# Kernel tuning notes

Measured on AMD Instinct MI355X. Metric: run time of the kernel, lower is better.

The kernel has to match this reference:

```python
import jax, jax.numpy as jnp
import numpy as np

K, T, CIN = 30000, 35, 7
EPS = 1e-5  # torch BatchNorm default


def _bn(x, gamma, beta):
    # x: [1, K, T, C]; per-channel batch-stat normalization over (0,1,2)
    mean = jnp.mean(x, axis=(0, 1, 2))
    var = jnp.var(x, axis=(0, 1, 2))
    return (x - mean) * jax.lax.rsqrt(var + EPS) * gamma + beta


def _vfe(x, mask, W, b, gamma, beta):
    # x: [1, K, T, Cin] -> [1, K, T, 2*units]
    pw = jnp.einsum('bkti,iu->bktu', x, W) + b
    pw = jax.nn.relu(_bn(pw, gamma, beta))
    agg = jnp.max(pw, axis=2, keepdims=True)            # [1, K, 1, units]
    out = jnp.concatenate([pw, jnp.broadcast_to(agg, pw.shape)], axis=-1)
    return out * mask


def setup_inputs() -> dict:
    key = jax.random.key(0)
    ks = jax.random.split(key, 8)
    inp = {}
    inp['x'] = jax.random.normal(ks[0], (K, T, CIN), jnp.float32)
    inp['coordinate'] = jax.random.randint(ks[1], (K, 4), 0, 1, dtype=jnp.int32)
    inp['batch_size'] = 1
    inp['W1'] = jax.random.normal(ks[2], (7, 16), jnp.float32) * 0.3
    inp['b1'] = jnp.zeros((16,), jnp.float32)
    inp['g1'] = jnp.ones((16,), jnp.float32)
    inp['be1'] = jnp.zeros((16,), jnp.float32)
    inp['W2'] = jax.random.normal(ks[3], (32, 64), jnp.float32) * 0.15
    inp['b2'] = jnp.zeros((64,), jnp.float32)
    inp['g2'] = jnp.ones((64,), jnp.float32)
    inp['be2'] = jnp.zeros((64,), jnp.float32)
    inp['Wd'] = jax.random.normal(ks[4], (128, 128), jnp.float32) * 0.1
    inp['bd'] = jnp.zeros((128,), jnp.float32)
    inp['gd'] = jnp.ones((128,), jnp.float32)
    inp['bed'] = jnp.zeros((128,), jnp.float32)
    return inp


def reference(x, coordinate, batch_size, W1, b1, g1, be1, W2, b2, g2, be2, Wd, bd, gd, bed):
    xb = x[None]                                   # [1, K, T, 7]
    # mask: 1 where the point's feature sum is nonzero
    mask = (jnp.sum(xb, axis=-1) != 0.0).astype(jnp.float32)[..., None]  # [1,K,T,1]
    h = _vfe(xb, mask, W1, b1, g1, be1)            # [1, K, T, 32]
    h = _vfe(h, mask, W2, b2, g2, be2)             # [1, K, T, 128]
    h = jnp.einsum('bktc,cd->bktd', h, Wd) + bd    # [1, K, T, 128]
    h = _bn(h, gd, bed)                            # BatchNorm2d after permute(0,3,1,2)
    h = jnp.where(h >= 0, h, 0.1 * h)              # leaky_relu(0.1)
    h = jnp.max(h, axis=2)                         # max over points -> [1, K, 128]
    out = jnp.transpose(h, (0, 2, 1))              # [1, 128, K] to match NCHW layout
    return (out, coordinate)
```

## Files before the change

### kernel.cpp

```cpp
#include <hip/hip_runtime.h>

#define KVOX 30000
#define TP 35
#define NPTS (KVOX * TP)
#define EPS_BN 1e-5f

typedef __attribute__((ext_vector_type(8))) short short8_t;
typedef __attribute__((ext_vector_type(4))) float f32x4;
typedef __attribute__((ext_vector_type(2))) float f32x2;

#define MFMA_BF16 __builtin_amdgcn_mfma_f32_16x16x32_bf16

#define SLOTG_OFF 0
#define SLOT2_OFF 2560
#define SLOT3_OFF 10752
#define PAR_A1 27136
#define PAR_C1 27152
#define PAR_A2 27168
#define PAR_C2 27232
#define PAR_A3 27296
#define PAR_C3 27424
#define STATS_FLOATS 27136
#define W2T_OFF 27552
#define WDT_OFF 28576
#define M3_OFF 36768
#define SMALL_FLOATS (36768 + KVOX * 64)
#define H1G_OFF SMALL_FLOATS
#define REC_DW 696
#define FULL_FLOATS (H1G_OFF + (KVOX / 2) * REC_DW)

__device__ __forceinline__ ushort f2bf(float f) {
    uint r;
    asm("v_cvt_pk_bf16_f32 %0, %1, %2" : "=v"(r) : "v"(f), "v"(f));
    return (ushort)r;
}
__device__ __forceinline__ uint f2bf2(float lo, float hi) {
    uint r;
    asm("v_cvt_pk_bf16_f32 %0, %1, %2" : "=v"(r) : "v"(lo), "v"(hi));
    return r;
}
__device__ __forceinline__ float bf2f(ushort h) {
    union { uint u; float f; } v; v.u = ((uint)h) << 16; return v.f;
}
__device__ __forceinline__ f32x2 mk2(float a, float b) {
    f32x2 r; r[0] = a; r[1] = b; return r;
}

__global__ __launch_bounds__(256) void k_prep_stats1(
    const float* __restrict__ x,
    const float* __restrict__ W2, const float* __restrict__ Wd,
    const float* __restrict__ gd,
    ushort* __restrict__ w2t, ushort* __restrict__ wdt,
    float* __restrict__ slotG) {
    if (blockIdx.x < 64) {
        int t = blockIdx.x * 256 + threadIdx.x;
        if (t < 2048) {
            int u = t >> 5, k = t & 31;
            w2t[t] = f2bf(W2[k * 64 + u]);
        }
        int u = t >> 7, k = t & 127;
        float sg = (gd[u] < 0.f) ? -1.f : 1.f;
        wdt[t] = f2bf(Wd[k * 128 + u] * sg);
        return;
    }
    int bid = blockIdx.x - 64;
    int tid = threadIdx.x;
    int gid = bid * 256 + tid;
    float sx[7], G[28];
#pragma unroll
    for (int c = 0; c < 7; ++c) sx[c] = 0.f;
#pragma unroll
    for (int i = 0; i < 28; ++i) G[i] = 0.f;
    for (int p = gid; p < NPTS; p += 256 * 256) {
        const float* xp = x + (size_t)p * 7;
        float xv[7];
#pragma unroll
        for (int c = 0; c < 7; ++c) { xv[c] = xp[c]; sx[c] += xv[c]; }
        int idx = 0;
#pragma unroll
        for (int i = 0; i < 7; ++i)
#pragma unroll
            for (int j = i; j < 7; ++j) { G[idx] = fmaf(xv[i], xv[j], G[idx]); ++idx; }
    }
    int lane = tid & 63;
    int wv = tid >> 6;
    int slot = (bid * 4 + wv) & 63;
#pragma unroll
    for (int k = 0; k < 35; ++k) {
        float v = (k < 28) ? G[k] : sx[k - 28];
#pragma unroll
        for (int m = 32; m > 0; m >>= 1) v += __shfl_xor(v, m, 64);
        if (lane == 0) atomicAdd(&slotG[slot * 40 + k], v);
    }
}

__global__ void k_affine1g(const float* __restrict__ slotG,
                           const float* __restrict__ W1, const float* __restrict__ b1,
                           const float* __restrict__ g1, const float* __restrict__ be1,
                           float* __restrict__ pa, float* __restrict__ pc, float invN) {
    __shared__ float red[35];
    int t = threadIdx.x;
    if (t < 35) {
        float s = 0.f;
#pragma unroll
        for (int sl = 0; sl < 64; ++sl) s += slotG[sl * 40 + t];
        red[t] = s;
    }
    __syncthreads();
    if (t < 16) {
        float wv[7];
#pragma unroll
        for (int c = 0; c < 7; ++c) wv[c] = W1[c * 16 + t];
        float b = b1[t];
        float sw = 0.f;
#pragma unroll
        for (int c = 0; c < 7; ++c) sw = fmaf(red[28 + c], wv[c], sw);
        float gq = 0.f;
        int idx = 0;
#pragma unroll
        for (int i = 0; i < 7; ++i)
#pragma unroll
            for (int j = i; j < 7; ++j) {
                float coef = wv[i] * wv[j];
                if (i != j) coef *= 2.f;
                gq = fmaf(coef, red[idx], gq);
                ++idx;
            }
        float mr = sw * invN;
        float mean = mr + b;
        float ex2 = gq * invN + 2.f * b * mr + b * b;
        float var = ex2 - mean * mean;
        float av = g1[t] * rsqrtf(var + EPS_BN);
        pa[t] = av;
        pc[t] = be1[t] - mean * av;
    }
}

__global__ void k_affine_b(const float* __restrict__ slots,
                           const float* __restrict__ g,
                           const float* __restrict__ be,
                           const float* __restrict__ bias,
                           float* __restrict__ pa, float* __restrict__ pc,
                           int C, float invN) {
    int u = threadIdx.x;
    if (u >= C) return;
    float s = 0.f, q = 0.f;
    for (int sl = 0; sl < 64; ++sl) {
        s += slots[sl * 2 * C + u];
        q += slots[sl * 2 * C + C + u];
    }
    float b = bias[u];
    float mr = s * invN;
    float mean = mr + b;
    float ex2 = q * invN + 2.f * b * mr + b * b;
    float var = ex2 - mean * mean;
    float av = g[u] * rsqrtf(var + EPS_BN);
    pa[u] = av;
    pc[u] = be[u] - mean * av;
}

__global__ void k_affine_b3(const float* __restrict__ slots,
                            const float* __restrict__ g,
                            const float* __restrict__ be,
                            const float* __restrict__ bias,
                            float* __restrict__ pa, float* __restrict__ pc,
                            int C, float invN) {
    int u = threadIdx.x;
    if (u >= C) return;
    float s = 0.f, q = 0.f;
    for (int sl = 0; sl < 64; ++sl) {
        s += slots[sl * 2 * C + u];
        q += slots[sl * 2 * C + C + u];
    }
    float sg = (g[u] < 0.f) ? -1.f : 1.f;
    s *= sg;
    float b = bias[u];
    float mr = s * invN;
    float mean = mr + b;
    float ex2 = q * invN + 2.f * b * mr + b * b;
    float var = ex2 - mean * mean;
    float av = g[u] * rsqrtf(var + EPS_BN);
    pa[u] = av;
    pc[u] = be[u] - mean * av;
}

__device__ __forceinline__ void phaseA_il(
    int k0, int tid,
    const float* __restrict__ x,
    const float* __restrict__ W1, const float* __restrict__ b1,
    const float* __restrict__ a1, const float* __restrict__ c1,
    ushort* __restrict__ h1, float* __restrict__ lmask,
    float* __restrict__ aggp, ushort* __restrict__ agg1bf) {
    int u = tid & 15;
    int g = tid >> 4;
    int v = g & 1;
    int th = g >> 1;
    float pmax = 0.f;
    if (th < 7) {
        float b1u = b1[u];
        float a1u = a1[u], c1u = c1[u];
        float w1c[7];
#pragma unroll
        for (int c = 0; c < 7; ++c) w1c[c] = W1[c * 16 + u];
#pragma unroll
        for (int i = 0; i < 5; ++i) {
            int t = th * 5 + i;
            const float* xp = x + ((size_t)(k0 + v) * TP + t) * 7;
            float xv[7];
            float sum7 = 0.f;
#pragma unroll
            for (int c = 0; c < 7; ++c) { xv[c] = xp[c]; sum7 += xv[c]; }
            float mkv = (sum7 != 0.f) ? 1.f : 0.f;
            int row = 2 * t + v;
            if (u == 0) lmask[row] = mkv;
            float val = b1u;
#pragma unroll
            for (int c = 0; c < 7; ++c) val = fmaf(xv[c], w1c[c], val);
            val = fmaxf(fmaf(a1u, val, c1u), 0.f);
            pmax = fmaxf(pmax, val);
            h1[row * 24 + u] = f2bf(val * mkv);
        }
    } else if (g < 16) {
#pragma unroll
        for (int i = 0; i < 5; ++i) {
            int row = 70 + (g & 1) + 2 * i;
            h1[row * 24 + u] = 0;
            if (u == 0) lmask[row] = 0.f;
        }
    }
    pmax = fmaxf(pmax, __shfl_xor(pmax, 32, 64));
    int w = tid >> 6;
    int lane = tid & 63;
    if (lane < 32 && w < 4) aggp[w * 32 + lane] = pmax;
    __syncthreads();
    if (tid < 16) {
        float g0 = fmaxf(fmaxf(aggp[u], aggp[32 + u]),
                         fmaxf(aggp[64 + u], aggp[96 + u]));
        float g1 = fmaxf(fmaxf(aggp[16 + u], aggp[48 + u]),
                         fmaxf(aggp[80 + u], aggp[112 + u]));
        agg1bf[u] = f2bf(g0);
        agg1bf[16 + u] = f2bf(g1);
    }
    __syncthreads();
}

template <bool DUMP>
__global__ __launch_bounds__(256, 8) void k_stats2(
    const float* __restrict__ x,
    const float* __restrict__ W1, const float* __restrict__ b1,
    const ushort* __restrict__ w2t,
    const float* __restrict__ ws,
    float* __restrict__ slot2, uint* __restrict__ recs) {
    __shared__ __align__(16) ushort h1[80 * 24];
    __shared__ float lmask[80];
    __shared__ float aggp[128];
    __shared__ __align__(16) ushort agg1bf[32];
    __shared__ __align__(16) uint zeros16[4];
    int tid = threadIdx.x;
    int k0 = blockIdx.x * 2;
    if (tid < 4) zeros16[tid] = 0;
    phaseA_il(k0, tid, x, W1, b1, ws + PAR_A1, ws + PAR_C1, h1, lmask, aggp, agg1bf);
    if (DUMP) {
        uint* rec = recs + (size_t)blockIdx.x * REC_DW;
        const uint* h1dw = (const uint*)h1;
        for (int i = tid; i < 640; i += 256) rec[i] = h1dw[(i >> 3) * 12 + (i & 7)];
        if (tid < 16) rec[640 + tid] = ((const uint*)agg1bf)[tid];
        if (tid < 40) rec[656 + tid] = f2bf2(lmask[2 * tid], lmask[2 * tid + 1]);
    }
    int w = tid >> 6, lane = tid & 63, lq = lane >> 4, lr = lane & 15;
    int u = w * 16 + lr;
    short8_t bB = *(const short8_t*)(w2t + u * 32 + (lq & 1) * 8);
    const ushort* pa = (lq < 2) ? (agg1bf + (lr & 1) * 16 + lq * 8) : (const ushort*)zeros16;
    short8_t pAf = *(const short8_t*)pa;
    short8_t bP = *(const short8_t*)(w2t + u * 32 + 16 + (lq & 1) * 8);
    f32x4 aP = {0.f, 0.f, 0.f, 0.f};
    aP = MFMA_BF16(pAf, bP, aP, 0, 0, 0);
    f32x2 p1p = mk2(__shfl(aP[0], lr, 64), __shfl(aP[1], lr, 64));
    f32x2 s1p = {0.f, 0.f}, s2p = {0.f, 0.f};
#pragma unroll
    for (int mt = 0; mt < 5; ++mt) {
        const ushort* ha = (lq < 2) ? (h1 + (mt * 16 + lr) * 24 + lq * 8) : (const ushort*)zeros16;
        short8_t af = *(const short8_t*)ha;
        f32x4 acc = {0.f, 0.f, 0.f, 0.f};
        acc = MFMA_BF16(af, bB, acc, 0, 0, 0);
        const f32x4 mk = *(const f32x4*)(lmask + mt * 16 + lq * 4);
        f32x2 am01 = (mk2(acc[0], acc[1]) + p1p) * mk2(mk[0], mk[1]);
        f32x2 am23 = (mk2(acc[2], acc[3]) + p1p) * mk2(mk[2], mk[3]);
        s1p += am01 + am23;
        s2p += am01 * am01;
        s2p += am23 * am23;
    }
    float s1 = s1p[0] + s1p[1], s2 = s2p[0] + s2p[1];
    s1 += __shfl_xor(s1, 16, 64); s1 += __shfl_xor(s1, 32, 64);
    s2 += __shfl_xor(s2, 16, 64); s2 += __shfl_xor(s2, 32, 64);
    if (lq == 0) {
        int slot = blockIdx.x & 63;
        atomicAdd(&slot2[slot * 128 + u], s1);
        atomicAdd(&slot2[slot * 128 + 64 + u], s2);
    }
}

__global__ __launch_bounds__(512, 8) void k_stage3_reuse(
    const uint* __restrict__ recs,
    const float* __restrict__ b2,
    const ushort* __restrict__ w2t, const ushort* __restrict__ wdt,
    const float* __restrict__ bd, const float* __restrict__ gd,
    const float* __restrict__ ws,
    float* __restrict__ slot3, ushort* __restrict__ m3) {
    __shared__ __align__(16) ushort h1[80 * 24];
    __shared__ __align__(16) ushort h2[80 * 72];
    __shared__ float lmask[80];
    __shared__ float aggh[2][2][64];
    __shared__ __align__(16) ushort agg1bf[32];
    __shared__ __align__(16) ushort agg2bf[2 * 64];
    __shared__ __align__(16) uint zeros16[4];
    int tid = threadIdx.x;
    int k0 = blockIdx.x * 2;
    int w = tid >> 6, lane = tid & 63, lq = lane >> 4, lr = lane & 15;

    {
        const uint* rec = recs + (size_t)blockIdx.x * REC_DW;
        uint* h1dw = (uint*)h1;
        h1dw[(tid >> 3) * 12 + (tid & 7)] = rec[tid];
        if (tid < 184) {
            int i2 = 512 + tid;
            if (i2 < 640) h1dw[(i2 >> 3) * 12 + (i2 & 7)] = rec[i2];
            else if (i2 < 656) ((uint*)agg1bf)[i2 - 640] = rec[i2];
            else {
                uint mw = rec[i2];
                int j = i2 - 656;
                lmask[2 * j] = bf2f((ushort)(mw & 0xffffu));
                lmask[2 * j + 1] = bf2f((ushort)(mw >> 16));
            }
        }
        if (tid < 4) zeros16[tid] = 0;
    }
    __syncthreads();

    {
        int mh = w >> 2, uq = w & 3;
        int u = uq * 16 + lr;
        short8_t bB = *(const short8_t*)(w2t + u * 32 + (lq & 1) * 8);
        const ushort* pa = (lq < 2) ? (agg1bf + (lr & 1) * 16 + lq * 8) : (const ushort*)zeros16;
        short8_t pAf = *(const short8_t*)pa;
        short8_t bP = *(const short8_t*)(w2t + u * 32 + 16 + (lq & 1) * 8);
        f32x4 aP = {0.f, 0.f, 0.f, 0.f};
        aP = MFMA_BF16(pAf, bP, aP, 0, 0, 0);
        f32x2 p1p = mk2(__shfl(aP[0], lr, 64), __shfl(aP[1], lr, 64));
        float a2u = ws[PAR_A2 + u];
        float c2u = fmaf(a2u, b2[u], ws[PAR_C2 + u]);
        f32x2 a2p = mk2(a2u, a2u), c2p = mk2(c2u, c2u);
        float av0 = 0.f, av1 = 0.f;
        int mt0 = mh ? 3 : 0, mt1 = mh ? 5 : 3;
        for (int mt = mt0; mt < mt1; ++mt) {
            const ushort* ha = (lq < 2) ? (h1 + (mt * 16 + lr) * 24 + lq * 8) : (const ushort*)zeros16;
            short8_t af = *(const short8_t*)ha;
            f32x4 acc = {0.f, 0.f, 0.f, 0.f};
            acc = MFMA_BF16(af, bB, acc, 0, 0, 0);
            const f32x4 mk = *(const f32x4*)(lmask + mt * 16 + lq * 4);
            int m0 = mt * 16 + lq * 4;
            f32x2 am01 = (mk2(acc[0], acc[1]) + p1p) * mk2(mk[0], mk[1]);
            f32x2 am23 = (mk2(acc[2], acc[3]) + p1p) * mk2(mk[2], mk[3]);
            f32x2 t01 = a2p * am01 + c2p;
            f32x2 t23 = a2p * am23 + c2p;
            float v0 = fmaxf(t01[0], 0.f), v1 = fmaxf(t01[1], 0.f);
            float v2 = fmaxf(t23[0], 0.f), v3 = fmaxf(t23[1], 0.f);
            h2[(m0 + 0) * 72 + u] = f2bf(v0);
            h2[(m0 + 1) * 72 + u] = f2bf(v1);
            h2[(m0 + 2) * 72 + u] = f2bf(v2);
            h2[(m0 + 3) * 72 + u] = f2bf(v3);
            if (mt == 4) {
                bool c01 = lq < 2, c23 = lq < 1;
                v0 = c01 ? v0 : 0.f; v1 = c01 ? v1 : 0.f;
                v2 = c23 ? v2 : 0.f; v3 = c23 ? v3 : 0.f;
            }
            av0 = fmaxf(av0, fmaxf(v0, v2));
            av1 = fmaxf(av1, fmaxf(v1, v3));
        }
        av0 = fmaxf(av0, __shfl_xor(av0, 16, 64));
        av0 = fmaxf(av0, __shfl_xor(av0, 32, 64));
        av1 = fmaxf(av1, __shfl_xor(av1, 16, 64));
        av1 = fmaxf(av1, __shfl_xor(av1, 32, 64));
        if (lq == 0) { aggh[mh][0][u] = av0; aggh[mh][1][u] = av1; }
    }
    __syncthreads();
    if (tid < 32) {
        int u2 = tid;
        float l0 = fmaxf(aggh[0][0][2 * u2], aggh[1][0][2 * u2]);
        float h0 = fmaxf(aggh[0][0][2 * u2 + 1], aggh[1][0][2 * u2 + 1]);
        float l1 = fmaxf(aggh[0][1][2 * u2], aggh[1][1][2 * u2]);
        float h1v = fmaxf(aggh[0][1][2 * u2 + 1], aggh[1][1][2 * u2 + 1]);
        ((uint*)agg2bf)[u2] = f2bf2(l0, h0);
        ((uint*)agg2bf)[32 + u2] = f2bf2(l1, h1v);
    }
    __syncthreads();

    {
        int u = w * 16 + lr;
        short8_t bM0 = *(const short8_t*)(wdt + u * 128 + lq * 8);
        short8_t bM1 = *(const short8_t*)(wdt + u * 128 + 32 + lq * 8);
        short8_t bP0 = *(const short8_t*)(wdt + u * 128 + 64 + lq * 8);
        short8_t bP1 = *(const short8_t*)(wdt + u * 128 + 96 + lq * 8);
        short8_t pA0 = *(const short8_t*)(agg2bf + (lr & 1) * 64 + lq * 8);
        short8_t pA1 = *(const short8_t*)(agg2bf + (lr & 1) * 64 + 32 + lq * 8);
        f32x4 aP = {0.f, 0.f, 0.f, 0.f};
        aP = MFMA_BF16(pA0, bP0, aP, 0, 0, 0);
        aP = MFMA_BF16(pA1, bP1, aP, 0, 0, 0);
        f32x2 p2p = mk2(__shfl(aP[0], lr, 64), __shfl(aP[1], lr, 64));
        float mx0 = -1e30f, mx1 = -1e30f;
        f32x2 s1p = {0.f, 0.f}, s2p = {0.f, 0.f};
#pragma unroll
        for (int mt = 0; mt < 5; ++mt) {
            const ushort* hrow = h2 + (mt * 16 + lr) * 72;
            short8_t a0 = *(const short8_t*)(hrow + lq * 8);
            short8_t a1 = *(const short8_t*)(hrow + 32 + lq * 8);
            f32x4 acc = {0.f, 0.f, 0.f, 0.f};
            acc = MFMA_BF16(a0, bM0, acc, 0, 0, 0);
            acc = MFMA_BF16(a1, bM1, acc, 0, 0, 0);
            const f32x4 mk = *(const f32x4*)(lmask + mt * 16 + lq * 4);
            f32x2 am01 = (mk2(acc[0], acc[1]) + p2p) * mk2(mk[0], mk[1]);
            f32x2 am23 = (mk2(acc[2], acc[3]) + p2p) * mk2(mk[2], mk[3]);
            s1p += am01 + am23;
            s2p += am01 * am01;
            s2p += am23 * am23;
            if (mt < 4) {
                mx0 = fmaxf(mx0, fmaxf(am01[0], am23[0]));
                mx1 = fmaxf(mx1, fmaxf(am01[1], am23[1]));
            } else {
                bool c01 = lq < 2, c23 = lq < 1;
                mx0 = fmaxf(mx0, fmaxf(c01 ? am01[0] : -1e30f, c23 ? am23[0] : -1e30f));
                mx1 = fmaxf(mx1, fmaxf(c01 ? am01[1] : -1e30f, c23 ? am23[1] : -1e30f));
            }
        }
        mx0 = fmaxf(mx0, __shfl_xor(mx0, 16, 64));
        mx0 = fmaxf(mx0, __shfl_xor(mx0, 32, 64));
        mx1 = fmaxf(mx1, __shfl_xor(mx1, 16, 64));
        mx1 = fmaxf(mx1, __shfl_xor(mx1, 32, 64));
        float s1 = s1p[0] + s1p[1], s2 = s2p[0] + s2p[1];
        s1 += __shfl_xor(s1, 16, 64); s1 += __shfl_xor(s1, 32, 64);
        s2 += __shfl_xor(s2, 16, 64); s2 += __shfl_xor(s2, 32, 64);
        if (lq == 0) {
            float sg = (gd[u] < 0.f) ? -1.f : 1.f;
            float bdu = bd[u];
            m3[(size_t)k0 * 128 + u] = f2bf(fmaf(sg, mx0, bdu));
            m3[(size_t)(k0 + 1) * 128 + u] = f2bf(fmaf(sg, mx1, bdu));
            int slot = blockIdx.x & 63;
            atomicAdd(&slot3[slot * 256 + u], s1);
            atomicAdd(&slot3[slot * 256 + 128 + u], s2);
        }
    }
}

__device__ __forceinline__ void phaseA_leg(
    int k0, int tid,
    const float* __restrict__ x,
    const float* __restrict__ W1, const float* __restrict__ b1,
    const float* __restrict__ a1, const float* __restrict__ c1,
    ushort* __restrict__ h1, float* __restrict__ lmask, float* __restrict__ aggp) {
    int u = tid & 15;
    int g = tid >> 4;
    int v = g & 1;
    int th = g >> 1;
    float pmax = 0.f;
    if (th < 7) {
        float b1u = b1[u];
        float a1u = a1[u], c1u = c1[u];
        float w1c[7];
#pragma unroll
        for (int c = 0; c < 7; ++c) w1c[c] = W1[c * 16 + u];
#pragma unroll
        for (int i = 0; i < 5; ++i) {
            int t = th * 5 + i;
            const float* xp = x + ((size_t)(k0 + v) * TP + t) * 7;
            float xv[7];
            float sum7 = 0.f;
#pragma unroll
            for (int c = 0; c < 7; ++c) { xv[c] = xp[c]; sum7 += xv[c]; }
            float mkv = (sum7 != 0.f) ? 1.f : 0.f;
            if (u == 0) lmask[v * TP + t] = mkv;
            float val = b1u;
#pragma unroll
            for (int c = 0; c < 7; ++c) val = fmaf(xv[c], w1c[c], val);
            val = fmaxf(fmaf(a1u, val, c1u), 0.f);
            pmax = fmaxf(pmax, val);
            h1[(v * TP + t) * 40 + u] = f2bf(val * mkv);
        }
    } else {
#pragma unroll
        for (int i = 0; i < 5; ++i) {
            int row = 70 + (g & 1) * 5 + i;
            h1[row * 40 + u] = 0;
            if (u == 0) lmask[row] = 0.f;
        }
    }
    pmax = fmaxf(pmax, __shfl_xor(pmax, 32, 64));
    int w = tid >> 6;
    int lane = tid & 63;
    if (lane < 32) aggp[w * 32 + lane] = pmax;
    __syncthreads();
    {
        int uu = tid & 15;
        int r0 = tid >> 4;
        float g0 = fmaxf(fmaxf(aggp[uu], aggp[32 + uu]),
                         fmaxf(aggp[64 + uu], aggp[96 + uu]));
        float g1 = fmaxf(fmaxf(aggp[16 + uu], aggp[48 + uu]),
                         fmaxf(aggp[80 + uu], aggp[112 + uu]));
        ushort a0 = f2bf(g0), a1b = f2bf(g1);
#pragma unroll
        for (int j = 0; j < 5; ++j) {
            int row = r0 + j * 16;
            float mkv = lmask[row];
            h1[row * 40 + 16 + uu] = (mkv != 0.f) ? ((row < TP) ? a0 : a1b) : (ushort)0;
        }
    }
    __syncthreads();
}

template <bool WSPATH>
__global__ __launch_bounds__(256) void k_stage3_full(
    const float* __restrict__ x,
    const float* __restrict__ W1, const float* __restrict__ b1,
    const float* __restrict__ b2,
    const ushort* __restrict__ w2t, const ushort* __restrict__ wdt,
    const float* __restrict__ bd, const float* __restrict__ gd,
    const float* __restrict__ ws,
    float* __restrict__ slot3,
    ushort* __restrict__ m3, float* __restrict__ outbuf) {
    __shared__ __align__(16) ushort h1[80 * 40];
    __shared__ __align__(16) ushort h2[80 * 136];
    __shared__ float lmask[80];
    __shared__ float aggp[128];
    __shared__ ushort agg2bf[128];
    int tid = threadIdx.x;
    int k0 = blockIdx.x * 2;
    int w = tid >> 6, lane = tid & 63, lq = lane >> 4, lr = lane & 15;
    phaseA_leg(k0, tid, x, W1, b1, ws + PAR_A1, ws + PAR_C1, h1, lmask, aggp);

    int u0 = w * 32;
    short8_t bfr[2][4];
#pragma unroll
    for (int s = 0; s < 2; ++s)
#pragma unroll
        for (int kk = 0; kk < 4; ++kk)
            bfr[s][kk] = *(const short8_t*)(wdt + ((u0 + s * 16 + lr) * 128 + kk * 32 + lq * 8));

    {
        int u = w * 16 + lr;
        short8_t bfrag = *(const short8_t*)(w2t + u * 32 + lq * 8);
        float a2u = ws[PAR_A2 + u];
        float c2p = fmaf(a2u, b2[u], ws[PAR_C2 + u]);
        float aggv0 = 0.f, aggv1 = 0.f;
#pragma unroll
        for (int mt = 0; mt < 5; ++mt) {
            short8_t afrag = *(const short8_t*)(h1 + (mt * 16 + lr) * 40 + lq * 8);
            f32x4 acc = {0.f, 0.f, 0.f, 0.f};
            acc = MFMA_BF16(afrag, bfrag, acc, 0, 0, 0);
#pragma unroll
            for (int r = 0; r < 4; ++r) {
                int m = mt * 16 + lq * 4 + r;
                float val = fmaxf(fmaf(a2u, acc[r], c2p), 0.f);
                float vm = (m < 70) ? val : 0.f;
                if (m < TP) aggv0 = fmaxf(aggv0, vm); else aggv1 = fmaxf(aggv1, vm);
                h2[m * 136 + u] = f2bf(val * lmask[m]);
            }
        }
        aggv0 = fmaxf(aggv0, __shfl_xor(aggv0, 16, 64));
        aggv0 = fmaxf(aggv0, __shfl_xor(aggv0, 32, 64));
        aggv1 = fmaxf(aggv1, __shfl_xor(aggv1, 16, 64));
        aggv1 = fmaxf(aggv1, __shfl_xor(aggv1, 32, 64));
        if (lq == 0) {
            agg2bf[u] = f2bf(aggv0);
            agg2bf[64 + u] = f2bf(aggv1);
        }
    }
    __syncthreads();
    {
        int c = tid & 63;
        int r0 = tid >> 6;
        ushort a0 = agg2bf[c], a1v = agg2bf[64 + c];
#pragma unroll
        for (int j = 0; j < 20; ++j) {
            int row = r0 + j * 4;
            float mkv = lmask[row];
            h2[row * 136 + 64 + c] = (mkv != 0.f) ? ((row < TP) ? a0 : a1v) : (ushort)0;
        }
    }
    __syncthreads();
    {
        float mxa[2][2], s1a[2], s2a[2];
#pragma unroll
        for (int s = 0; s < 2; ++s) {
            s1a[s] = 0.f; s2a[s] = 0.f;
            mxa[s][0] = -1e30f; mxa[s][1] = -1e30f;
        }
#pragma unroll
        for (int mt = 0; mt < 5; ++mt) {
            short8_t af[4];
#pragma unroll
            for (int kk = 0; kk < 4; ++kk)
                af[kk] = *(const short8_t*)(h2 + (mt * 16 + lr) * 136 + kk * 32 + lq * 8);
#pragma unroll
            for (int s = 0; s < 2; ++s) {
                f32x4 acc = {0.f, 0.f, 0.f, 0.f};
#pragma unroll
                for (int kk = 0; kk < 4; ++kk)
                    acc = MFMA_BF16(af[kk], bfr[s][kk], acc, 0, 0, 0);
#pragma unroll
                for (int r = 0; r < 4; ++r) {
                    float a = acc[r];
                    s1a[s] += a;
                    s2a[s] = fmaf(a, a, s2a[s]);
                    int m = mt * 16 + lq * 4 + r;
                    if (mt <= 1) mxa[s][0] = fmaxf(mxa[s][0], a);
                    else if (mt == 3) mxa[s][1] = fmaxf(mxa[s][1], a);
                    else if (mt == 2) { if (m < TP) mxa[s][0] = fmaxf(mxa[s][0], a); else mxa[s][1] = fmaxf(mxa[s][1], a); }
                    else { if (m < 70) mxa[s][1] = fmaxf(mxa[s][1], a); }
                }
            }
        }
#pragma unroll
        for (int s = 0; s < 2; ++s) {
#pragma unroll
            for (int v = 0; v < 2; ++v) {
                mxa[s][v] = fmaxf(mxa[s][v], __shfl_xor(mxa[s][v], 16, 64));
                mxa[s][v] = fmaxf(mxa[s][v], __shfl_xor(mxa[s][v], 32, 64));
            }
            s1a[s] += __shfl_xor(s1a[s], 16, 64); s1a[s] += __shfl_xor(s1a[s], 32, 64);
            s2a[s] += __shfl_xor(s2a[s], 16, 64); s2a[s] += __shfl_xor(s2a[s], 32, 64);
        }
        if (lq == 0) {
            int slot = blockIdx.x & 63;
#pragma unroll
            for (int s = 0; s < 2; ++s) {
                int u = u0 + s * 16 + lr;
                float bdu = bd[u];
                float sg = (gd[u] < 0.f) ? -1.f : 1.f;
#pragma unroll
                for (int v = 0; v < 2; ++v) {
                    float res = fmaf(sg, mxa[s][v], bdu);
                    if (WSPATH) m3[(size_t)(k0 + v) * 128 + u] = f2bf(res);
                    else        outbuf[(size_t)u * KVOX + (k0 + v)] = res;
                }
                atomicAdd(&slot3[slot * 256 + u], s1a[s]);
                atomicAdd(&slot3[slot * 256 + 128 + u], s2a[s]);
            }
        }
    }
}

__global__ __launch_bounds__(256) void k_final_ws(const ushort* __restrict__ m3,
                                                  const float* __restrict__ ws,
                                                  float* __restrict__ out) {
    __shared__ float tile[32][33];
    int tx = threadIdx.x & 31;
    int ty = threadIdx.x >> 5;
    int v0 = blockIdx.x * 32;
    int u0 = blockIdx.y * 32;
    const float* a3 = ws + PAR_A3;
    const float* c3 = ws + PAR_C3;
#pragma unroll
    for (int r = ty; r < 32; r += 8) {
        int v = v0 + r, u = u0 + tx;
        float y = 0.f;
        if (v < KVOX) {
            float a = a3[u], c = c3[u];
            float val = bf2f(m3[(size_t)v * 128 + u]);
            y = a * val + c;
            y = (y >= 0.f) ? y : 0.1f * y;
        }
        tile[r][tx] = y;
    }
    __syncthreads();
#pragma unroll
    for (int r = ty; r < 32; r += 8) {
        int u = u0 + r, v = v0 + tx;
        if (v < KVOX) out[(size_t)u * KVOX + v] = tile[tx][r];
    }
}

__global__ __launch_bounds__(256) void k_final_inplace(const float* __restrict__ ws,
                                                       float* __restrict__ out) {
    int v = blockIdx.x * 256 + threadIdx.x;
    int u = blockIdx.y;
    if (v >= KVOX) return;
    float a = ws[PAR_A3 + u], c = ws[PAR_C3 + u];
    size_t idx = (size_t)u * KVOX + v;
    float y = a * out[idx] + c;
    out[idx] = (y >= 0.f) ? y : 0.1f * y;
}

extern "C" void kernel_launch(void* const* d_in, const int* in_sizes, int n_in,
                              void* d_out, int out_size, void* d_ws, size_t ws_size,
                              hipStream_t stream) {
    const float* x   = (const float*)d_in[0];
    const void*  coord = d_in[1];
    const float* W1  = (const float*)d_in[3];
    const float* b1  = (const float*)d_in[4];
    const float* g1  = (const float*)d_in[5];
    const float* be1 = (const float*)d_in[6];
    const float* W2  = (const float*)d_in[7];
    const float* b2  = (const float*)d_in[8];
    const float* g2  = (const float*)d_in[9];
    const float* be2 = (const float*)d_in[10];
    const float* Wd  = (const float*)d_in[11];
    const float* bd  = (const float*)d_in[12];
    const float* gd  = (const float*)d_in[13];
    const float* bed = (const float*)d_in[14];
    float* ws = (float*)d_ws;
    float* out = (float*)d_out;
    ushort* w2t = (ushort*)(ws + W2T_OFF);
    ushort* wdt = (ushort*)(ws + WDT_OFF);
    ushort* m3  = (ushort*)(ws + M3_OFF);
    uint* recs  = (uint*)(ws + H1G_OFF);

    size_t wsf = ws_size / 4;
    bool full = wsf >= (size_t)FULL_FLOATS;
    bool small = wsf >= (size_t)SMALL_FLOATS;
    const float invN = 1.f / (float)NPTS;

    hipMemsetAsync(d_ws, 0, (size_t)STATS_FLOATS * 4, stream);

    k_prep_stats1<<<64 + 256, 256, 0, stream>>>(x, W2, Wd, gd, w2t, wdt, ws + SLOTG_OFF);
    k_affine1g<<<1, 64, 0, stream>>>(ws + SLOTG_OFF, W1, b1, g1, be1, ws + PAR_A1, ws + PAR_C1, invN);
    if (full)
        k_stats2<true><<<KVOX / 2, 256, 0, stream>>>(x, W1, b1, w2t, ws, ws + SLOT2_OFF, recs);
    else
        k_stats2<false><<<KVOX / 2, 256, 0, stream>>>(x, W1, b1, w2t, ws, ws + SLOT2_OFF, recs);
    k_affine_b<<<1, 64, 0, stream>>>(ws + SLOT2_OFF, g2, be2, b2, ws + PAR_A2, ws + PAR_C2, 64, invN);

    if (full) {
        k_stage3_reuse<<<KVOX / 2, 512, 0, stream>>>(recs, b2, w2t, wdt, bd, gd, ws,
                                                     ws + SLOT3_OFF, m3);
        k_affine_b3<<<1, 128, 0, stream>>>(ws + SLOT3_OFF, gd, bed, bd, ws + PAR_A3, ws + PAR_C3, 128, invN);
        k_final_ws<<<dim3((KVOX + 31) / 32, 4), 256, 0, stream>>>(m3, ws, out);
    } else if (small) {
        k_stage3_full<true><<<KVOX / 2, 256, 0, stream>>>(x, W1, b1, b2, w2t, wdt, bd, gd, ws,
                                                          ws + SLOT3_OFF, m3, out);
        k_affine_b3<<<1, 128, 0, stream>>>(ws + SLOT3_OFF, gd, bed, bd, ws + PAR_A3, ws + PAR_C3, 128, invN);
        k_final_ws<<<dim3((KVOX + 31) / 32, 4), 256, 0, stream>>>(m3, ws, out);
    } else {
        k_stage3_full<false><<<KVOX / 2, 256, 0, stream>>>(x, W1, b1, b2, w2t, wdt, bd, gd, ws,
                                                           ws + SLOT3_OFF, m3, out);
        k_affine_b3<<<1, 128, 0, stream>>>(ws + SLOT3_OFF, gd, bed, bd, ws + PAR_A3, ws + PAR_C3, 128, invN);
        k_final_inplace<<<dim3((KVOX + 255) / 256, 128), 256, 0, stream>>>(ws, out);
    }
    hipMemcpyAsync((char*)d_out + (size_t)128 * KVOX * 4, coord,
                   (size_t)KVOX * 4 * sizeof(int), hipMemcpyDeviceToDevice, stream);
}
```

Before: 176.3 us.

## Process four voxels per block in stats2 and stage3 with full MFMA row use

Blocks in k_stats2 and k_stage3_reuse now handle four voxels (140 point rows padded to 144) instead of two. Each 16x16 MFMA tile therefore fills all four accumulator lanes rather than two, and the number of blocks is halved. The per-voxel max aggregation in stage 3 now goes through shared-memory atomicMax on float bits instead of a two-step reduction. Separately, the first-stage Gram statistics loop loads x as 16-byte vectors covering four points at once. The costs are larger shared-memory use per block, a bigger record layout, and reliance on the maxima being non-negative after ReLU so that atomicMax on float bits orders correctly.

```diff
diff --git a/kernel.cpp b/kernel.cpp
--- a/kernel.cpp
+++ b/kernel.cpp
@@ -7,7 +7,6 @@
 
 typedef __attribute__((ext_vector_type(8))) short short8_t;
 typedef __attribute__((ext_vector_type(4))) float f32x4;
-typedef __attribute__((ext_vector_type(2))) float f32x2;
 
 #define MFMA_BF16 __builtin_amdgcn_mfma_f32_16x16x32_bf16
 
@@ -26,8 +25,8 @@
 #define M3_OFF 36768
 #define SMALL_FLOATS (36768 + KVOX * 64)
 #define H1G_OFF SMALL_FLOATS
-#define REC_DW 696
-#define FULL_FLOATS (H1G_OFF + (KVOX / 2) * REC_DW)
+#define REC_DW 1224
+#define FULL_FLOATS (H1G_OFF + (KVOX / 4) * REC_DW)
 
 __device__ __forceinline__ ushort f2bf(float f) {
     uint r;
@@ -41,9 +40,6 @@
 }
 __device__ __forceinline__ float bf2f(ushort h) {
     union { uint u; float f; } v; v.u = ((uint)h) << 16; return v.f;
-}
-__device__ __forceinline__ f32x2 mk2(float a, float b) {
-    f32x2 r; r[0] = a; r[1] = b; return r;
 }
 
 __global__ __launch_bounds__(256) void k_prep_stats1(
@@ -71,16 +67,26 @@
     for (int c = 0; c < 7; ++c) sx[c] = 0.f;
 #pragma unroll
     for (int i = 0; i < 28; ++i) G[i] = 0.f;
-    for (int p = gid; p < NPTS; p += 256 * 256) {
-        const float* xp = x + (size_t)p * 7;
-        float xv[7];
-#pragma unroll
-        for (int c = 0; c < 7; ++c) { xv[c] = xp[c]; sx[c] += xv[c]; }
-        int idx = 0;
-#pragma unroll
-        for (int i = 0; i < 7; ++i)
-#pragma unroll
-            for (int j = i; j < 7; ++j) { G[idx] = fmaf(xv[i], xv[j], G[idx]); ++idx; }
+    for (size_t p4 = (size_t)gid * 4; p4 < NPTS; p4 += (size_t)65536 * 4) {
+        const f32x4* xp = (const f32x4*)(x + p4 * 7);
+        f32x4 q[7];
+#pragma unroll
+        for (int c = 0; c < 7; ++c) q[c] = xp[c];
+#pragma unroll
+        for (int j = 0; j < 4; ++j) {
+            float xv[7];
+#pragma unroll
+            for (int c = 0; c < 7; ++c) {
+                int idx = j * 7 + c;
+                xv[c] = q[idx >> 2][idx & 3];
+                sx[c] += xv[c];
+            }
+            int idx = 0;
+#pragma unroll
+            for (int i = 0; i < 7; ++i)
+#pragma unroll
+                for (int jj = i; jj < 7; ++jj) { G[idx] = fmaf(xv[i], xv[jj], G[idx]); ++idx; }
+        }
     }
     int lane = tid & 63;
     int wv = tid >> 6;
@@ -184,17 +190,17 @@
     pc[u] = be[u] - mean * av;
 }
 
-__device__ __forceinline__ void phaseA_il(
+__device__ __forceinline__ void phaseA4(
     int k0, int tid,
     const float* __restrict__ x,
     const float* __restrict__ W1, const float* __restrict__ b1,
     const float* __restrict__ a1, const float* __restrict__ c1,
     ushort* __restrict__ h1, float* __restrict__ lmask,
-    float* __restrict__ aggp, ushort* __restrict__ agg1bf) {
+    float* __restrict__ aggp , ushort* __restrict__ agg1bf ) {
     int u = tid & 15;
     int g = tid >> 4;
-    int v = g & 1;
-    int th = g >> 1;
+    int v = g & 3;
+    int th = g >> 2;
     float pmax = 0.f;
     if (th < 7) {
         float b1u = b1[u];
@@ -211,7 +217,7 @@
 #pragma unroll
             for (int c = 0; c < 7; ++c) { xv[c] = xp[c]; sum7 += xv[c]; }
             float mkv = (sum7 != 0.f) ? 1.f : 0.f;
-            int row = 2 * t + v;
+            int row = 4 * t + v;
             if (u == 0) lmask[row] = mkv;
             float val = b1u;
 #pragma unroll
@@ -220,77 +226,73 @@
             pmax = fmaxf(pmax, val);
             h1[row * 24 + u] = f2bf(val * mkv);
         }
-    } else if (g < 16) {
-#pragma unroll
-        for (int i = 0; i < 5; ++i) {
-            int row = 70 + (g & 1) + 2 * i;
-            h1[row * 24 + u] = 0;
-            if (u == 0) lmask[row] = 0.f;
-        }
-    }
-    pmax = fmaxf(pmax, __shfl_xor(pmax, 32, 64));
+    } else {
+        int row = 140 + v;
+        h1[row * 24 + u] = 0;
+        if (u == 0) lmask[row] = 0.f;
+    }
     int w = tid >> 6;
     int lane = tid & 63;
-    if (lane < 32 && w < 4) aggp[w * 32 + lane] = pmax;
-    __syncthreads();
-    if (tid < 16) {
-        float g0 = fmaxf(fmaxf(aggp[u], aggp[32 + u]),
-                         fmaxf(aggp[64 + u], aggp[96 + u]));
-        float g1 = fmaxf(fmaxf(aggp[16 + u], aggp[48 + u]),
-                         fmaxf(aggp[80 + u], aggp[112 + u]));
-        agg1bf[u] = f2bf(g0);
-        agg1bf[16 + u] = f2bf(g1);
+    if (w < 7) aggp[w * 64 + lane] = pmax;
+    __syncthreads();
+    if (tid < 64) {
+        float m = aggp[tid];
+#pragma unroll
+        for (int ww = 1; ww < 7; ++ww) m = fmaxf(m, aggp[ww * 64 + tid]);
+        agg1bf[tid] = f2bf(m);
     }
     __syncthreads();
 }
 
 template <bool DUMP>
-__global__ __launch_bounds__(256, 8) void k_stats2(
+__global__ __launch_bounds__(512, 8) void k_stats2(
     const float* __restrict__ x,
     const float* __restrict__ W1, const float* __restrict__ b1,
     const ushort* __restrict__ w2t,
     const float* __restrict__ ws,
     float* __restrict__ slot2, uint* __restrict__ recs) {
-    __shared__ __align__(16) ushort h1[80 * 24];
-    __shared__ float lmask[80];
-    __shared__ float aggp[128];
-    __shared__ __align__(16) ushort agg1bf[32];
+    __shared__ __align__(16) ushort h1[144 * 24];
+    __shared__ float lmask[144];
+    __shared__ float aggp[7 * 64];
+    __shared__ __align__(16) ushort agg1bf[64];
     __shared__ __align__(16) uint zeros16[4];
     int tid = threadIdx.x;
-    int k0 = blockIdx.x * 2;
+    int k0 = blockIdx.x * 4;
     if (tid < 4) zeros16[tid] = 0;
-    phaseA_il(k0, tid, x, W1, b1, ws + PAR_A1, ws + PAR_C1, h1, lmask, aggp, agg1bf);
+    phaseA4(k0, tid, x, W1, b1, ws + PAR_A1, ws + PAR_C1, h1, lmask, aggp, agg1bf);
     if (DUMP) {
         uint* rec = recs + (size_t)blockIdx.x * REC_DW;
         const uint* h1dw = (const uint*)h1;
-        for (int i = tid; i < 640; i += 256) rec[i] = h1dw[(i >> 3) * 12 + (i & 7)];
-        if (tid < 16) rec[640 + tid] = ((const uint*)agg1bf)[tid];
-        if (tid < 40) rec[656 + tid] = f2bf2(lmask[2 * tid], lmask[2 * tid + 1]);
+        for (int i = tid; i < 1120; i += 512) rec[i] = h1dw[(i >> 3) * 12 + (i & 7)];
+        if (tid < 32) rec[1120 + tid] = ((const uint*)agg1bf)[tid];
+        if (tid < 70) rec[1152 + tid] = f2bf2(lmask[2 * tid], lmask[2 * tid + 1]);
     }
     int w = tid >> 6, lane = tid & 63, lq = lane >> 4, lr = lane & 15;
-    int u = w * 16 + lr;
+    int mh = w >> 2, uq = w & 3;
+    int u = uq * 16 + lr;
     short8_t bB = *(const short8_t*)(w2t + u * 32 + (lq & 1) * 8);
-    const ushort* pa = (lq < 2) ? (agg1bf + (lr & 1) * 16 + lq * 8) : (const ushort*)zeros16;
-    short8_t pAf = *(const short8_t*)pa;
     short8_t bP = *(const short8_t*)(w2t + u * 32 + 16 + (lq & 1) * 8);
+    const ushort* pap = (lq < 2) ? (agg1bf + (lr & 3) * 16 + (lq & 1) * 8) : (const ushort*)zeros16;
+    short8_t pAf = *(const short8_t*)pap;
     f32x4 aP = {0.f, 0.f, 0.f, 0.f};
     aP = MFMA_BF16(pAf, bP, aP, 0, 0, 0);
-    f32x2 p1p = mk2(__shfl(aP[0], lr, 64), __shfl(aP[1], lr, 64));
-    f32x2 s1p = {0.f, 0.f}, s2p = {0.f, 0.f};
-#pragma unroll
-    for (int mt = 0; mt < 5; ++mt) {
-        const ushort* ha = (lq < 2) ? (h1 + (mt * 16 + lr) * 24 + lq * 8) : (const ushort*)zeros16;
+    f32x4 p1;
+    p1[0] = __shfl(aP[0], lr, 64); p1[1] = __shfl(aP[1], lr, 64);
+    p1[2] = __shfl(aP[2], lr, 64); p1[3] = __shfl(aP[3], lr, 64);
+    f32x4 s1p = {0.f, 0.f, 0.f, 0.f}, s2p = {0.f, 0.f, 0.f, 0.f};
+    int mt0 = mh ? 5 : 0, mt1 = mh ? 9 : 5;
+    for (int mt = mt0; mt < mt1; ++mt) {
+        const ushort* ha = (lq < 2) ? (h1 + (mt * 16 + lr) * 24 + (lq & 1) * 8) : (const ushort*)zeros16;
         short8_t af = *(const short8_t*)ha;
         f32x4 acc = {0.f, 0.f, 0.f, 0.f};
         acc = MFMA_BF16(af, bB, acc, 0, 0, 0);
-        const f32x4 mk = *(const f32x4*)(lmask + mt * 16 + lq * 4);
-        f32x2 am01 = (mk2(acc[0], acc[1]) + p1p) * mk2(mk[0], mk[1]);
-        f32x2 am23 = (mk2(acc[2], acc[3]) + p1p) * mk2(mk[2], mk[3]);
-        s1p += am01 + am23;
-        s2p += am01 * am01;
-        s2p += am23 * am23;
-    }
-    float s1 = s1p[0] + s1p[1], s2 = s2p[0] + s2p[1];
+        f32x4 mk = *(const f32x4*)(lmask + mt * 16 + lq * 4);
+        f32x4 am = (acc + p1) * mk;
+        s1p += am;
+        s2p += am * am;
+    }
+    float s1 = s1p[0] + s1p[1] + s1p[2] + s1p[3];
+    float s2 = s2p[0] + s2p[1] + s2p[2] + s2p[3];
     s1 += __shfl_xor(s1, 16, 64); s1 += __shfl_xor(s1, 32, 64);
     s2 += __shfl_xor(s2, 16, 64); s2 += __shfl_xor(s2, 32, 64);
     if (lq == 0) {
@@ -307,33 +309,38 @@
     const float* __restrict__ bd, const float* __restrict__ gd,
     const float* __restrict__ ws,
     float* __restrict__ slot3, ushort* __restrict__ m3) {
-    __shared__ __align__(16) ushort h1[80 * 24];
-    __shared__ __align__(16) ushort h2[80 * 72];
-    __shared__ float lmask[80];
-    __shared__ float aggh[2][2][64];
-    __shared__ __align__(16) ushort agg1bf[32];
-    __shared__ __align__(16) ushort agg2bf[2 * 64];
+    __shared__ __align__(16) ushort h1[144 * 24];
+    __shared__ __align__(16) ushort h2[144 * 72];
+    __shared__ float lmask[144];
+    __shared__ __align__(16) uint aggfU[4 * 68];
+    __shared__ __align__(16) ushort agg1bf[64];
     __shared__ __align__(16) uint zeros16[4];
     int tid = threadIdx.x;
-    int k0 = blockIdx.x * 2;
+    int k0 = blockIdx.x * 4;
     int w = tid >> 6, lane = tid & 63, lq = lane >> 4, lr = lane & 15;
 
     {
         const uint* rec = recs + (size_t)blockIdx.x * REC_DW;
         uint* h1dw = (uint*)h1;
-        h1dw[(tid >> 3) * 12 + (tid & 7)] = rec[tid];
-        if (tid < 184) {
-            int i2 = 512 + tid;
-            if (i2 < 640) h1dw[(i2 >> 3) * 12 + (i2 & 7)] = rec[i2];
-            else if (i2 < 656) ((uint*)agg1bf)[i2 - 640] = rec[i2];
-            else {
-                uint mw = rec[i2];
-                int j = i2 - 656;
-                lmask[2 * j] = bf2f((ushort)(mw & 0xffffu));
-                lmask[2 * j + 1] = bf2f((ushort)(mw >> 16));
-            }
-        }
-        if (tid < 4) zeros16[tid] = 0;
+        {
+            int i = tid;              h1dw[(i >> 3) * 12 + (i & 7)] = rec[i];
+            i = tid + 512;            h1dw[(i >> 3) * 12 + (i & 7)] = rec[i];
+            i = tid + 1024; if (i < 1120) h1dw[(i >> 3) * 12 + (i & 7)] = rec[i];
+        }
+        if (tid < 48) h1dw[140 * 12 + tid] = 0u;
+        if (tid < 32) ((uint*)agg1bf)[tid] = rec[1120 + tid];
+        if (tid < 72) {
+            if (tid < 70) {
+                uint mw = rec[1152 + tid];
+                lmask[2 * tid] = bf2f((ushort)(mw & 0xffffu));
+                lmask[2 * tid + 1] = bf2f((ushort)(mw >> 16));
+            } else {
+                int j = 140 + (tid - 70) * 2;
+                lmask[j] = 0.f; lmask[j + 1] = 0.f;
+            }
+        }
+        if (tid < 272) aggfU[tid] = 0u;
+        if (tid < 4) zeros16[tid] = 0u;
     }
     __syncthreads();
 
@@ -341,57 +348,48 @@
         int mh = w >> 2, uq = w & 3;
         int u = uq * 16 + lr;
         short8_t bB = *(const short8_t*)(w2t + u * 32 + (lq & 1) * 8);
-        const ushort* pa = (lq < 2) ? (agg1bf + (lr & 1) * 16 + lq * 8) : (const ushort*)zeros16;
-        short8_t pAf = *(const short8_t*)pa;
         short8_t bP = *(const short8_t*)(w2t + u * 32 + 16 + (lq & 1) * 8);
+        const ushort* pap = (lq < 2) ? (agg1bf + (lr & 3) * 16 + (lq & 1) * 8) : (const ushort*)zeros16;
+        short8_t pAf = *(const short8_t*)pap;
         f32x4 aP = {0.f, 0.f, 0.f, 0.f};
         aP = MFMA_BF16(pAf, bP, aP, 0, 0, 0);
-        f32x2 p1p = mk2(__shfl(aP[0], lr, 64), __shfl(aP[1], lr, 64));
+        f32x4 p1;
+        p1[0] = __shfl(aP[0], lr, 64); p1[1] = __shfl(aP[1], lr, 64);
+        p1[2] = __shfl(aP[2], lr, 64); p1[3] = __shfl(aP[3], lr, 64);
         float a2u = ws[PAR_A2 + u];
         float c2u = fmaf(a2u, b2[u], ws[PAR_C2 + u]);
-        f32x2 a2p = mk2(a2u, a2u), c2p = mk2(c2u, c2u);
-        float av0 = 0.f, av1 = 0.f;
-        int mt0 = mh ? 3 : 0, mt1 = mh ? 5 : 3;
+        f32x4 av = {0.f, 0.f, 0.f, 0.f};
+        int mt0 = mh ? 5 : 0, mt1 = mh ? 9 : 5;
         for (int mt = mt0; mt < mt1; ++mt) {
-            const ushort* ha = (lq < 2) ? (h1 + (mt * 16 + lr) * 24 + lq * 8) : (const ushort*)zeros16;
+            const ushort* ha = (lq < 2) ? (h1 + (mt * 16 + lr) * 24 + (lq & 1) * 8) : (const ushort*)zeros16;
             short8_t af = *(const short8_t*)ha;
             f32x4 acc = {0.f, 0.f, 0.f, 0.f};
             acc = MFMA_BF16(af, bB, acc, 0, 0, 0);
-            const f32x4 mk = *(const f32x4*)(lmask + mt * 16 + lq * 4);
+            f32x4 mk = *(const f32x4*)(lmask + mt * 16 + lq * 4);
             int m0 = mt * 16 + lq * 4;
-            f32x2 am01 = (mk2(acc[0], acc[1]) + p1p) * mk2(mk[0], mk[1]);
-            f32x2 am23 = (mk2(acc[2], acc[3]) + p1p) * mk2(mk[2], mk[3]);
-            f32x2 t01 = a2p * am01 + c2p;
-            f32x2 t23 = a2p * am23 + c2p;
-            float v0 = fmaxf(t01[0], 0.f), v1 = fmaxf(t01[1], 0.f);
-            float v2 = fmaxf(t23[0], 0.f), v3 = fmaxf(t23[1], 0.f);
-            h2[(m0 + 0) * 72 + u] = f2bf(v0);
-            h2[(m0 + 1) * 72 + u] = f2bf(v1);
-            h2[(m0 + 2) * 72 + u] = f2bf(v2);
-            h2[(m0 + 3) * 72 + u] = f2bf(v3);
-            if (mt == 4) {
-                bool c01 = lq < 2, c23 = lq < 1;
-                v0 = c01 ? v0 : 0.f; v1 = c01 ? v1 : 0.f;
-                v2 = c23 ? v2 : 0.f; v3 = c23 ? v3 : 0.f;
-            }
-            av0 = fmaxf(av0, fmaxf(v0, v2));
-            av1 = fmaxf(av1, fmaxf(v1, v3));
-        }
-        av0 = fmaxf(av0, __shfl_xor(av0, 16, 64));
-        av0 = fmaxf(av0, __shfl_xor(av0, 32, 64));
-        av1 = fmaxf(av1, __shfl_xor(av1, 16, 64));
-        av1 = fmaxf(av1, __shfl_xor(av1, 32, 64));
-        if (lq == 0) { aggh[mh][0][u] = av0; aggh[mh][1][u] = av1; }
-    }
-    __syncthreads();
-    if (tid < 32) {
-        int u2 = tid;
-        float l0 = fmaxf(aggh[0][0][2 * u2], aggh[1][0][2 * u2]);
-        float h0 = fmaxf(aggh[0][0][2 * u2 + 1], aggh[1][0][2 * u2 + 1]);
-        float l1 = fmaxf(aggh[0][1][2 * u2], aggh[1][1][2 * u2]);
-        float h1v = fmaxf(aggh[0][1][2 * u2 + 1], aggh[1][1][2 * u2 + 1]);
-        ((uint*)agg2bf)[u2] = f2bf2(l0, h0);
-        ((uint*)agg2bf)[32 + u2] = f2bf2(l1, h1v);
+            f32x4 vals;
+#pragma unroll
+            for (int r = 0; r < 4; ++r) {
+                float am = (acc[r] + p1[r]) * mk[r];
+                float val = fmaxf(fmaf(a2u, am, c2u), 0.f);
+                h2[(m0 + r) * 72 + u] = f2bf(val);
+                vals[r] = val;
+            }
+            if (!(mt == 8 && lq == 3)) {
+#pragma unroll
+                for (int r = 0; r < 4; ++r) av[r] = fmaxf(av[r], vals[r]);
+            }
+        }
+#pragma unroll
+        for (int r = 0; r < 4; ++r) {
+            av[r] = fmaxf(av[r], __shfl_xor(av[r], 16, 64));
+            av[r] = fmaxf(av[r], __shfl_xor(av[r], 32, 64));
+        }
+        if (lq == 0) {
+#pragma unroll
+            for (int r = 0; r < 4; ++r)
+                atomicMax(&aggfU[r * 68 + u], __float_as_uint(av[r]));
+        }
     }
     __syncthreads();
 
@@ -401,49 +399,59 @@
         short8_t bM1 = *(const short8_t*)(wdt + u * 128 + 32 + lq * 8);
         short8_t bP0 = *(const short8_t*)(wdt + u * 128 + 64 + lq * 8);
         short8_t bP1 = *(const short8_t*)(wdt + u * 128 + 96 + lq * 8);
-        short8_t pA0 = *(const short8_t*)(agg2bf + (lr & 1) * 64 + lq * 8);
-        short8_t pA1 = *(const short8_t*)(agg2bf + (lr & 1) * 64 + 32 + lq * 8);
+        const float* aggf = (const float*)aggfU;
+        f32x4 q0 = *(const f32x4*)(aggf + (lr & 3) * 68 + lq * 8);
+        f32x4 q1 = *(const f32x4*)(aggf + (lr & 3) * 68 + lq * 8 + 4);
+        f32x4 q2 = *(const f32x4*)(aggf + (lr & 3) * 68 + 32 + lq * 8);
+        f32x4 q3 = *(const f32x4*)(aggf + (lr & 3) * 68 + 32 + lq * 8 + 4);
+        union { uint uu[4]; short8_t s8; } pc0, pc1;
+        pc0.uu[0] = f2bf2(q0[0], q0[1]); pc0.uu[1] = f2bf2(q0[2], q0[3]);
+        pc0.uu[2] = f2bf2(q1[0], q1[1]); pc0.uu[3] = f2bf2(q1[2], q1[3]);
+        pc1.uu[0] = f2bf2(q2[0], q2[1]); pc1.uu[1] = f2bf2(q2[2], q2[3]);
+        pc1.uu[2] = f2bf2(q3[0], q3[1]); pc1.uu[3] = f2bf2(q3[2], q3[3]);
         f32x4 aP = {0.f, 0.f, 0.f, 0.f};
-        aP = MFMA_BF16(pA0, bP0, aP, 0, 0, 0);
-        aP = MFMA_BF16(pA1, bP1, aP, 0, 0, 0);
-        f32x2 p2p = mk2(__shfl(aP[0], lr, 64), __shfl(aP[1], lr, 64));
-        float mx0 = -1e30f, mx1 = -1e30f;
-        f32x2 s1p = {0.f, 0.f}, s2p = {0.f, 0.f};
-#pragma unroll
-        for (int mt = 0; mt < 5; ++mt) {
+        aP = MFMA_BF16(pc0.s8, bP0, aP, 0, 0, 0);
+        aP = MFMA_BF16(pc1.s8, bP1, aP, 0, 0, 0);
+        f32x4 p2;
+        p2[0] = __shfl(aP[0], lr, 64); p2[1] = __shfl(aP[1], lr, 64);
+        p2[2] = __shfl(aP[2], lr, 64); p2[3] = __shfl(aP[3], lr, 64);
+        f32x4 s1p = {0.f, 0.f, 0.f, 0.f}, s2p = {0.f, 0.f, 0.f, 0.f};
+        f32x4 mx = {-1e30f, -1e30f, -1e30f, -1e30f};
+#pragma unroll
+        for (int mt = 0; mt < 9; ++mt) {
             const ushort* hrow = h2 + (mt * 16 + lr) * 72;
             short8_t a0 = *(const short8_t*)(hrow + lq * 8);
             short8_t a1 = *(const short8_t*)(hrow + 32 + lq * 8);
             f32x4 acc = {0.f, 0.f, 0.f, 0.f};
             acc = MFMA_BF16(a0, bM0, acc, 0, 0, 0);
             acc = MFMA_BF16(a1, bM1, acc, 0, 0, 0);
-            const f32x4 mk = *(const f32x4*)(lmask + mt * 16 + lq * 4);
-            f32x2 am01 = (mk2(acc[0], acc[1]) + p2p) * mk2(mk[0], mk[1]);
-            f32x2 am23 = (mk2(acc[2], acc[3]) + p2p) * mk2(mk[2], mk[3]);
-            s1p += am01 + am23;
-            s2p += am01 * am01;
-            s2p += am23 * am23;
-            if (mt < 4) {
-                mx0 = fmaxf(mx0, fmaxf(am01[0], am23[0]));
-                mx1 = fmaxf(mx1, fmaxf(am01[1], am23[1]));
-            } else {
-                bool c01 = lq < 2, c23 = lq < 1;
-                mx0 = fmaxf(mx0, fmaxf(c01 ? am01[0] : -1e30f, c23 ? am23[0] : -1e30f));
-                mx1 = fmaxf(mx1, fmaxf(c01 ? am01[1] : -1e30f, c23 ? am23[1] : -1e30f));
-            }
-        }
-        mx0 = fmaxf(mx0, __shfl_xor(mx0, 16, 64));
-        mx0 = fmaxf(mx0, __shfl_xor(mx0, 32, 64));
-        mx1 = fmaxf(mx1, __shfl_xor(mx1, 16, 64));
-        mx1 = fmaxf(mx1, __shfl_xor(mx1, 32, 64));
-        float s1 = s1p[0] + s1p[1], s2 = s2p[0] + s2p[1];
+            f32x4 mk = *(const f32x4*)(lmask + mt * 16 + lq * 4);
+            f32x4 am = (acc + p2) * mk;
+            s1p += am;
+            s2p += am * am;
+            if (mt < 8) {
+#pragma unroll
+                for (int r = 0; r < 4; ++r) mx[r] = fmaxf(mx[r], am[r]);
+            } else if (lq < 3) {
+#pragma unroll
+                for (int r = 0; r < 4; ++r) mx[r] = fmaxf(mx[r], am[r]);
+            }
+        }
+#pragma unroll
+        for (int r = 0; r < 4; ++r) {
+            mx[r] = fmaxf(mx[r], __shfl_xor(mx[r], 16, 64));
+            mx[r] = fmaxf(mx[r], __shfl_xor(mx[r], 32, 64));
+        }
+        float s1 = s1p[0] + s1p[1] + s1p[2] + s1p[3];
+        float s2 = s2p[0] + s2p[1] + s2p[2] + s2p[3];
         s1 += __shfl_xor(s1, 16, 64); s1 += __shfl_xor(s1, 32, 64);
         s2 += __shfl_xor(s2, 16, 64); s2 += __shfl_xor(s2, 32, 64);
         if (lq == 0) {
             float sg = (gd[u] < 0.f) ? -1.f : 1.f;
             float bdu = bd[u];
-            m3[(size_t)k0 * 128 + u] = f2bf(fmaf(sg, mx0, bdu));
-            m3[(size_t)(k0 + 1) * 128 + u] = f2bf(fmaf(sg, mx1, bdu));
+#pragma unroll
+            for (int r = 0; r < 4; ++r)
+                m3[(size_t)(k0 + r) * 128 + u] = f2bf(fmaf(sg, mx[r], bdu));
             int slot = blockIdx.x & 63;
             atomicAdd(&slot3[slot * 256 + u], s1);
             atomicAdd(&slot3[slot * 256 + 128 + u], s2);
@@ -723,13 +731,13 @@
     k_prep_stats1<<<64 + 256, 256, 0, stream>>>(x, W2, Wd, gd, w2t, wdt, ws + SLOTG_OFF);
     k_affine1g<<<1, 64, 0, stream>>>(ws + SLOTG_OFF, W1, b1, g1, be1, ws + PAR_A1, ws + PAR_C1, invN);
     if (full)
-        k_stats2<true><<<KVOX / 2, 256, 0, stream>>>(x, W1, b1, w2t, ws, ws + SLOT2_OFF, recs);
+        k_stats2<true><<<KVOX / 4, 512, 0, stream>>>(x, W1, b1, w2t, ws, ws + SLOT2_OFF, recs);
     else
-        k_stats2<false><<<KVOX / 2, 256, 0, stream>>>(x, W1, b1, w2t, ws, ws + SLOT2_OFF, recs);
+        k_stats2<false><<<KVOX / 4, 512, 0, stream>>>(x, W1, b1, w2t, ws, ws + SLOT2_OFF, recs);
     k_affine_b<<<1, 64, 0, stream>>>(ws + SLOT2_OFF, g2, be2, b2, ws + PAR_A2, ws + PAR_C2, 64, invN);
 
     if (full) {
-        k_stage3_reuse<<<KVOX / 2, 512, 0, stream>>>(recs, b2, w2t, wdt, bd, gd, ws,
+        k_stage3_reuse<<<KVOX / 4, 512, 0, stream>>>(recs, b2, w2t, wdt, bd, gd, ws,
                                                      ws + SLOT3_OFF, m3);
         k_affine_b3<<<1, 128, 0, stream>>>(ws + SLOT3_OFF, gd, bed, bd, ws + PAR_A3, ws + PAR_C3, 128, invN);
         k_final_ws<<<dim3((KVOX + 31) / 32, 4), 256, 0, stream>>>(m3, ws, out);
```

After: 154.0 us. 1.14x faster.
